# Kernel optimization log

Measured on AMD Instinct MI355X. Metric: run time of the kernel, lower is better.

Reference implementation:

```python
import jax, jax.numpy as jnp
import numpy as np

MARGIN = 0.3
EPS = 1e-12


def setup_inputs() -> dict:
    key = jax.random.key(0)
    k1, k2 = jax.random.split(key)
    inputs = jax.random.normal(k1, (256, 2048), dtype=jnp.float32)
    targets = jax.random.randint(k2, (256,), 0, 32, dtype=jnp.int64)
    return {"inputs": inputs, "targets": targets}


def reference(inputs, targets):
    # Pairwise Euclidean distance matrix [n, n] via GEMM.
    sq = jnp.sum(inputs * inputs, axis=1)                      # [n]
    dist = sq[:, None] + sq[None, :] - 2.0 * (inputs @ inputs.T)
    dist = jnp.sqrt(jnp.clip(dist, EPS, None))                 # [n, n]

    same = targets[:, None] == targets[None, :]                # [n, n]
    # Triplet margin for all (anchor, positive, negative) in one broadcast.
    tri = dist[:, :, None] - dist[:, None, :] + MARGIN         # [n, n, n]
    tri = jnp.clip(tri, EPS, None)
    # Valid: same label for (a, p), different label for (a, neg).
    valid = same[:, :, None] & (~same)[:, None, :]             # [n, n, n]
    # Torch version stacks only valid triplets (dynamic shape); here we
    # return the dense [n, n, n] tensor with invalid entries zeroed.
    return jnp.where(valid, tri, 0.0)
```

## Files before the change

kernel.cpp:

```cpp
#include <hip/hip_runtime.h>

#define N 256
#define D 2048
#define MARGIN_F 0.3f
#define EPS_F 1e-12f

__global__ __launch_bounds__(64) void sq_kernel(const float* __restrict__ x,
                                                float* __restrict__ sq) {
    int row = blockIdx.x;
    int lane = threadIdx.x;
    const float4* xr = (const float4*)(x + (size_t)row * D);
    float acc = 0.f;
#pragma unroll
    for (int it = 0; it < 8; ++it) {
        float4 v = xr[lane + 64 * it];
        acc += v.x * v.x + v.y * v.y + v.z * v.z + v.w * v.w;
    }
#pragma unroll
    for (int off = 32; off > 0; off >>= 1) acc += __shfl_down(acc, off, 64);
    if (lane == 0) sq[row] = acc;
}

__global__ __launch_bounds__(256, 1) void gram_kernel(const float* __restrict__ x,
                                                      float* __restrict__ part) {
    __shared__ __align__(16) float As[128 * 32];
    __shared__ __align__(16) float Bs[128 * 32];
    const int bi = blockIdx.x, bj = blockIdx.y, ks = blockIdx.z;
    const int i0 = bi * 128, j0 = bj * 128, k0 = ks * 32;
    const int tid = threadIdx.x;

#pragma unroll
    for (int it = 0; it < 4; ++it) {
        int f = tid + 256 * it;
        int row = f >> 3;
        int c4 = f & 7;
        int sc4 = c4 ^ ((row >> 3) & 7);
        float4 va = *(const float4*)(x + (size_t)(i0 + row) * D + k0 + c4 * 4);
        float4 vb = *(const float4*)(x + (size_t)(j0 + row) * D + k0 + c4 * 4);
        *(float4*)(As + row * 32 + sc4 * 4) = va;
        *(float4*)(Bs + row * 32 + sc4 * 4) = vb;
    }
    __syncthreads();

    const int tx = tid & 15;
    const int ty = tid >> 4;
    float acc[8][8];
#pragma unroll
    for (int r = 0; r < 8; ++r)
#pragma unroll
        for (int c = 0; c < 8; ++c) acc[r][c] = 0.f;

#pragma unroll
    for (int k4 = 0; k4 < 8; ++k4) {
        float4 a[8], b[8];
#pragma unroll
        for (int r = 0; r < 8; ++r) {
            int ia = ty * 8 + r;
            int ib = tx * 8 + r;
            a[r] = *(const float4*)(As + ia * 32 + ((k4 ^ ((ia >> 3) & 7)) << 2));
            b[r] = *(const float4*)(Bs + ib * 32 + ((k4 ^ ((ib >> 3) & 7)) << 2));
        }
#pragma unroll
        for (int r = 0; r < 8; ++r)
#pragma unroll
            for (int c = 0; c < 8; ++c)
                acc[r][c] += a[r].x * b[c].x + a[r].y * b[c].y +
                             a[r].z * b[c].z + a[r].w * b[c].w;
    }

    float* pout = part + (size_t)ks * (N * N);
#pragma unroll
    for (int r = 0; r < 8; ++r) {
        int gi = i0 + ty * 8 + r;
#pragma unroll
        for (int c = 0; c < 8; c += 4) {
            float4 v = make_float4(acc[r][c], acc[r][c + 1], acc[r][c + 2], acc[r][c + 3]);
            *(float4*)(pout + (size_t)gi * N + j0 + tx * 8 + c) = v;
        }
    }
}

__global__ __launch_bounds__(64) void reduce_kernel(const float* __restrict__ part,
                                                    const float* __restrict__ sq,
                                                    float* __restrict__ dist) {
    int t = blockIdx.x * 64 + threadIdx.x;
    float4 acc = make_float4(0.f, 0.f, 0.f, 0.f);
#pragma unroll 8
    for (int ks = 0; ks < 64; ++ks) {
        float4 v = *(const float4*)(part + (size_t)ks * (N * N) + (size_t)t * 4);
        acc.x += v.x; acc.y += v.y; acc.z += v.z; acc.w += v.w;
    }
    int i = t >> 6;
    int j4 = (t & 63) * 4;
    float si = sq[i];
    float4 sj = *(const float4*)(sq + j4);
    float4 d;
    d.x = sqrtf(fmaxf(si + sj.x - 2.f * acc.x, EPS_F));
    d.y = sqrtf(fmaxf(si + sj.y - 2.f * acc.y, EPS_F));
    d.z = sqrtf(fmaxf(si + sj.z - 2.f * acc.z, EPS_F));
    d.w = sqrtf(fmaxf(si + sj.w - 2.f * acc.w, EPS_F));
    *(float4*)(dist + (size_t)t * 4) = d;
}

__global__ __launch_bounds__(256) void triplet_kernel(const float* __restrict__ dist,
                                                      const int* __restrict__ targets,
                                                      float* __restrict__ out) {
    __shared__ __align__(16) float drow[N];
    __shared__ int lab[N];
    const int a = blockIdx.x;
    const int p0 = blockIdx.y * 16;
    const int tid = threadIdx.x;
    lab[tid] = targets[tid];
    drow[tid] = dist[a * N + tid];
    __syncthreads();

    const int la = lab[a];
    const int lane = tid & 63;
    const int pq = tid >> 6;

    float4 dan = *(const float4*)(drow + lane * 4);
    float4 mb = make_float4(MARGIN_F - dan.x, MARGIN_F - dan.y,
                            MARGIN_F - dan.z, MARGIN_F - dan.w);
    float nok_x = (lab[lane * 4 + 0] != la) ? 1.f : 0.f;
    float nok_y = (lab[lane * 4 + 1] != la) ? 1.f : 0.f;
    float nok_z = (lab[lane * 4 + 2] != la) ? 1.f : 0.f;
    float nok_w = (lab[lane * 4 + 3] != la) ? 1.f : 0.f;

    float* obase = out + ((size_t)a << 16) + lane * 4;
#pragma unroll
    for (int j = 0; j < 4; ++j) {
        int p = p0 + pq * 4 + j;
        float4 r;
        if (lab[p] == la) {
            float dap = drow[p];
            r.x = fmaxf(dap + mb.x, EPS_F) * nok_x;
            r.y = fmaxf(dap + mb.y, EPS_F) * nok_y;
            r.z = fmaxf(dap + mb.z, EPS_F) * nok_z;
            r.w = fmaxf(dap + mb.w, EPS_F) * nok_w;
        } else {
            r = make_float4(0.f, 0.f, 0.f, 0.f);
        }
        *(float4*)(obase + (size_t)p * N) = r;
    }
}

extern "C" void kernel_launch(void* const* d_in, const int* in_sizes, int n_in,
                              void* d_out, int out_size, void* d_ws, size_t ws_size,
                              hipStream_t stream) {
    const float* x = (const float*)d_in[0];
    const int* targets = (const int*)d_in[1];
    float* out = (float*)d_out;
    float* ws = (float*)d_ws;

    float* sq = ws;
    float* dist = ws + 256;
    size_t need = (size_t)(256 + N * N + 64 * N * N) * sizeof(float);
    float* part = (ws_size >= need) ? (ws + 256 + N * N) : (float*)d_out;

    sq_kernel<<<256, 64, 0, stream>>>(x, sq);
    gram_kernel<<<dim3(2, 2, 64), 256, 0, stream>>>(x, part);
    reduce_kernel<<<256, 64, 0, stream>>>(part, sq, dist);
    triplet_kernel<<<dim3(256, 16), 256, 0, stream>>>(dist, targets, out);
}
```

Before: 98.96 us.

## Store split-K partials in fp16 and fuse reduction into triplet kernel

Split-K GEMM partial sums are now written as half precision, which halves the partial-buffer traffic. The reduction and distance computation move into the triplet kernel, removing one launch and the dist round trip. Output stores become nontemporal. Rounding the partial dot products to fp16 loses precision in the distances, which may break tolerance. Each (a, y) block recomputes its distance row, so that reduction work is duplicated twice.

```diff
diff --git a/kernel.cpp b/kernel.cpp
--- a/kernel.cpp
+++ b/kernel.cpp
@@ -1,9 +1,12 @@
 #include <hip/hip_runtime.h>
+#include <hip/hip_fp16.h>
 
 #define N 256
 #define D 2048
 #define MARGIN_F 0.3f
 #define EPS_F 1e-12f
+
+typedef float v4f __attribute__((ext_vector_type(4)));
 
 __global__ __launch_bounds__(64) void sq_kernel(const float* __restrict__ x,
                                                 float* __restrict__ sq) {
@@ -22,7 +25,7 @@
 }
 
 __global__ __launch_bounds__(256, 1) void gram_kernel(const float* __restrict__ x,
-                                                      float* __restrict__ part) {
+                                                      __half* __restrict__ part) {
     __shared__ __align__(16) float As[128 * 32];
     __shared__ __align__(16) float Bs[128 * 32];
     const int bi = blockIdx.x, bj = blockIdx.y, ks = blockIdx.z;
@@ -68,38 +71,77 @@
                              a[r].z * b[c].z + a[r].w * b[c].w;
     }
 
-    float* pout = part + (size_t)ks * (N * N);
+    __half* pout = part + (size_t)ks * (N * N);
 #pragma unroll
     for (int r = 0; r < 8; ++r) {
         int gi = i0 + ty * 8 + r;
-#pragma unroll
-        for (int c = 0; c < 8; c += 4) {
-            float4 v = make_float4(acc[r][c], acc[r][c + 1], acc[r][c + 2], acc[r][c + 3]);
-            *(float4*)(pout + (size_t)gi * N + j0 + tx * 8 + c) = v;
+        union { __half2 h2[4]; uint4 u; } pk;
+#pragma unroll
+        for (int c = 0; c < 4; ++c)
+            pk.h2[c] = __floats2half2_rn(acc[r][2 * c], acc[r][2 * c + 1]);
+        *(uint4*)(pout + (size_t)gi * N + j0 + tx * 8) = pk.u;
+    }
+}
+
+__global__ __launch_bounds__(256) void fused_kernel(const __half* __restrict__ part,
+                                                    const float* __restrict__ sq,
+                                                    const int* __restrict__ targets,
+                                                    float* __restrict__ out) {
+    __shared__ __align__(16) float drow[N];
+    __shared__ int lab[N];
+    const int a = blockIdx.x;
+    const int tid = threadIdx.x;
+    lab[tid] = targets[tid];
+
+    float dot = 0.f;
+    const __half* base = part + a * N + tid;
+#pragma unroll 8
+    for (int ks = 0; ks < 64; ++ks)
+        dot += __half2float(base[(size_t)ks * (N * N)]);
+    drow[tid] = sqrtf(fmaxf(sq[a] + sq[tid] - 2.f * dot, EPS_F));
+    __syncthreads();
+
+    const int la = lab[a];
+    const int lane = tid & 63;
+    const int pq = tid >> 6;
+    const int p0 = blockIdx.y * 128 + pq * 32;
+
+    v4f dan = *(const v4f*)(drow + lane * 4);
+    v4f mb = MARGIN_F - dan;
+    v4f nokv = {(lab[lane * 4 + 0] != la) ? 1.f : 0.f,
+                (lab[lane * 4 + 1] != la) ? 1.f : 0.f,
+                (lab[lane * 4 + 2] != la) ? 1.f : 0.f,
+                (lab[lane * 4 + 3] != la) ? 1.f : 0.f};
+
+    float* obase = out + ((size_t)a << 16) + lane * 4;
+#pragma unroll 4
+    for (int i = 0; i < 32; ++i) {
+        int p = p0 + i;
+        v4f r = {0.f, 0.f, 0.f, 0.f};
+        if (lab[p] == la) {
+            float dap = drow[p];
+            v4f t = dap + mb;
+            t.x = fmaxf(t.x, EPS_F);
+            t.y = fmaxf(t.y, EPS_F);
+            t.z = fmaxf(t.z, EPS_F);
+            t.w = fmaxf(t.w, EPS_F);
+            r = t * nokv;
         }
-    }
-}
-
-__global__ __launch_bounds__(64) void reduce_kernel(const float* __restrict__ part,
-                                                    const float* __restrict__ sq,
-                                                    float* __restrict__ dist) {
-    int t = blockIdx.x * 64 + threadIdx.x;
-    float4 acc = make_float4(0.f, 0.f, 0.f, 0.f);
+        __builtin_nontemporal_store(r, (v4f*)(obase + (size_t)p * N));
+    }
+}
+
+__global__ __launch_bounds__(256) void dist_kernel(const __half* __restrict__ part,
+                                                   const float* __restrict__ sq,
+                                                   float* __restrict__ dist) {
+    const int a = blockIdx.x;
+    const int tid = threadIdx.x;
+    float dot = 0.f;
+    const __half* base = part + a * N + tid;
 #pragma unroll 8
-    for (int ks = 0; ks < 64; ++ks) {
-        float4 v = *(const float4*)(part + (size_t)ks * (N * N) + (size_t)t * 4);
-        acc.x += v.x; acc.y += v.y; acc.z += v.z; acc.w += v.w;
-    }
-    int i = t >> 6;
-    int j4 = (t & 63) * 4;
-    float si = sq[i];
-    float4 sj = *(const float4*)(sq + j4);
-    float4 d;
-    d.x = sqrtf(fmaxf(si + sj.x - 2.f * acc.x, EPS_F));
-    d.y = sqrtf(fmaxf(si + sj.y - 2.f * acc.y, EPS_F));
-    d.z = sqrtf(fmaxf(si + sj.z - 2.f * acc.z, EPS_F));
-    d.w = sqrtf(fmaxf(si + sj.w - 2.f * acc.w, EPS_F));
-    *(float4*)(dist + (size_t)t * 4) = d;
+    for (int ks = 0; ks < 64; ++ks)
+        dot += __half2float(base[(size_t)ks * (N * N)]);
+    dist[a * N + tid] = sqrtf(fmaxf(sq[a] + sq[tid] - 2.f * dot, EPS_F));
 }
 
 __global__ __launch_bounds__(256) void triplet_kernel(const float* __restrict__ dist,
@@ -118,29 +160,28 @@
     const int lane = tid & 63;
     const int pq = tid >> 6;
 
-    float4 dan = *(const float4*)(drow + lane * 4);
-    float4 mb = make_float4(MARGIN_F - dan.x, MARGIN_F - dan.y,
-                            MARGIN_F - dan.z, MARGIN_F - dan.w);
-    float nok_x = (lab[lane * 4 + 0] != la) ? 1.f : 0.f;
-    float nok_y = (lab[lane * 4 + 1] != la) ? 1.f : 0.f;
-    float nok_z = (lab[lane * 4 + 2] != la) ? 1.f : 0.f;
-    float nok_w = (lab[lane * 4 + 3] != la) ? 1.f : 0.f;
+    v4f dan = *(const v4f*)(drow + lane * 4);
+    v4f mb = MARGIN_F - dan;
+    v4f nokv = {(lab[lane * 4 + 0] != la) ? 1.f : 0.f,
+                (lab[lane * 4 + 1] != la) ? 1.f : 0.f,
+                (lab[lane * 4 + 2] != la) ? 1.f : 0.f,
+                (lab[lane * 4 + 3] != la) ? 1.f : 0.f};
 
     float* obase = out + ((size_t)a << 16) + lane * 4;
 #pragma unroll
     for (int j = 0; j < 4; ++j) {
         int p = p0 + pq * 4 + j;
-        float4 r;
+        v4f r = {0.f, 0.f, 0.f, 0.f};
         if (lab[p] == la) {
             float dap = drow[p];
-            r.x = fmaxf(dap + mb.x, EPS_F) * nok_x;
-            r.y = fmaxf(dap + mb.y, EPS_F) * nok_y;
-            r.z = fmaxf(dap + mb.z, EPS_F) * nok_z;
-            r.w = fmaxf(dap + mb.w, EPS_F) * nok_w;
-        } else {
-            r = make_float4(0.f, 0.f, 0.f, 0.f);
+            v4f t = dap + mb;
+            t.x = fmaxf(t.x, EPS_F);
+            t.y = fmaxf(t.y, EPS_F);
+            t.z = fmaxf(t.z, EPS_F);
+            t.w = fmaxf(t.w, EPS_F);
+            r = t * nokv;
         }
-        *(float4*)(obase + (size_t)p * N) = r;
+        __builtin_nontemporal_store(r, (v4f*)(obase + (size_t)p * N));
     }
 }
 
@@ -153,12 +194,19 @@
     float* ws = (float*)d_ws;
 
     float* sq = ws;
-    float* dist = ws + 256;
-    size_t need = (size_t)(256 + N * N + 64 * N * N) * sizeof(float);
-    float* part = (ws_size >= need) ? (ws + 256 + N * N) : (float*)d_out;
-
-    sq_kernel<<<256, 64, 0, stream>>>(x, sq);
-    gram_kernel<<<dim3(2, 2, 64), 256, 0, stream>>>(x, part);
-    reduce_kernel<<<256, 64, 0, stream>>>(part, sq, dist);
-    triplet_kernel<<<dim3(256, 16), 256, 0, stream>>>(dist, targets, out);
-}
+    size_t need_full = 1024 + (size_t)64 * N * N * sizeof(__half) + 1024;
+
+    if (ws_size >= need_full) {
+        __half* part = (__half*)(ws + 256);
+        sq_kernel<<<256, 64, 0, stream>>>(x, sq);
+        gram_kernel<<<dim3(2, 2, 64), 256, 0, stream>>>(x, part);
+        fused_kernel<<<dim3(256, 2), 256, 0, stream>>>(part, sq, targets, out);
+    } else {
+        __half* part = (__half*)d_out;
+        float* dist = ws + 256;
+        sq_kernel<<<256, 64, 0, stream>>>(x, sq);
+        gram_kernel<<<dim3(2, 2, 64), 256, 0, stream>>>(x, part);
+        dist_kernel<<<256, 256, 0, stream>>>(part, sq, dist);
+        triplet_kernel<<<dim3(256, 16), 256, 0, stream>>>(dist, targets, out);
+    }
+}
```

Result: faster. 95.65 us (-3.3%).
